# Kernel tuning notes

Hardware: AMD Instinct MI355X
Metric: run time of the kernel (lower is better)

## Reference

```python
import jax, jax.numpy as jnp
import numpy as np

N = 100000
E = 3200000
F_IN = 512
NUM_CLASSES = 8
H1, C1 = 4, 8   # conv1: 4 heads, 8 channels each (concat -> 32)
H2, C2 = 1, NUM_CLASSES  # conv2: 1 head, mean (concat=False)
NEG_SLOPE = 0.2


def gat_conv(x, W, att_src, att_dst, bias, src, dst, num_nodes, concat):
    """PyG-style GATConv (eval mode, self-loops already in src/dst)."""
    H, C = att_src.shape
    xp = (x @ W).reshape(-1, H, C)              # [N, H, C]
    a_s = (xp * att_src[None]).sum(-1)           # [N, H]
    a_d = (xp * att_dst[None]).sum(-1)           # [N, H]
    e = jax.nn.leaky_relu(a_s[src] + a_d[dst], NEG_SLOPE)  # [E, H]
    # segment softmax over destination nodes (stable)
    e_max = jax.ops.segment_max(e, dst, num_segments=num_nodes)
    e = jnp.exp(e - e_max[dst])
    denom = jax.ops.segment_sum(e, dst, num_segments=num_nodes)
    alpha = e / denom[dst]                        # [E, H]
    msg = xp[src] * alpha[..., None]              # [E, H, C]
    out = jax.ops.segment_sum(msg, dst, num_segments=num_nodes)  # [N, H, C]
    if concat:
        out = out.reshape(num_nodes, H * C)
    else:
        out = out.mean(axis=1)
    return out + bias


def setup_inputs() -> dict:
    key = jax.random.key(0)
    ks = jax.random.split(key, 9)
    s = 0.1
    return {
        "x": jax.random.normal(ks[0], (N, F_IN), dtype=jnp.float32),
        "edge_index": jax.random.randint(ks[1], (2, E), 0, N, dtype=jnp.int32),
        "W1": jax.random.normal(ks[2], (F_IN, H1 * C1), dtype=jnp.float32) * s,
        "att_src1": jax.random.normal(ks[3], (H1, C1), dtype=jnp.float32) * s,
        "att_dst1": jax.random.normal(ks[4], (H1, C1), dtype=jnp.float32) * s,
        "b1": jnp.zeros((H1 * C1,), dtype=jnp.float32),
        "W2": jax.random.normal(ks[5], (H1 * C1, H2 * C2), dtype=jnp.float32) * s,
        "att_src2": jax.random.normal(ks[6], (H2, C2), dtype=jnp.float32) * s,
        "att_dst2": jax.random.normal(ks[7], (H2, C2), dtype=jnp.float32) * s,
        "b2": jnp.zeros((C2,), dtype=jnp.float32),
    }


def reference(x, edge_index, W1, att_src1, att_dst1, b1, W2, att_src2, att_dst2, b2):
    # PyG GATConv default add_self_loops=True
    loop = jnp.arange(N, dtype=edge_index.dtype)
    src = jnp.concatenate([edge_index[0], loop])
    dst = jnp.concatenate([edge_index[1], loop])
    # dropout is identity in eval mode
    h = jax.nn.elu(gat_conv(x, W1, att_src1, att_dst1, b1, src, dst, N, True))
    out = gat_conv(h, W2, att_src2, att_dst2, b2, src, dst, N, False)
    return out
```

## Files before the change

kernel.cpp:

```cpp
#include <hip/hip_runtime.h>

typedef unsigned short u16;
typedef unsigned int   u32;

#define NN  100000
#define EE  3200000
#define ETOT 3300000
#define FIN 512
#define NBUK 512
#define NPB  196
#define TILE_A 8192
#define NBLK_A ((ETOT + TILE_A - 1) / TILE_A)

typedef __attribute__((ext_vector_type(8))) short bfx8;
typedef __attribute__((ext_vector_type(4))) float f32x4;

__device__ __forceinline__ float bf2f(u16 u){ return __uint_as_float(((u32)u) << 16); }
__device__ __forceinline__ float lo16f(u32 v){ return __uint_as_float(v << 16); }
__device__ __forceinline__ float hi16f(u32 v){ return __uint_as_float(v & 0xffff0000u); }
__device__ __forceinline__ u16 f2bf(float f){
  u32 u = __float_as_uint(f);
  u += 0x7fffu + ((u >> 16) & 1u);
  return (u16)(u >> 16);
}
__device__ __forceinline__ u32 pack2(float a, float b){
  return ((u32)f2bf(b) << 16) | (u32)f2bf(a);
}


__global__ void __launch_bounds__(256) k_bcnt(const int* __restrict__ ei,
                                              u32* __restrict__ bcnt){
  __shared__ u32 h[NBUK];
  int t = threadIdx.x;
  h[t] = 0; h[t + 256] = 0;
  __syncthreads();
  int stride = gridDim.x * 256;
  for (int e = blockIdx.x*256 + t; e < ETOT; e += stride){
    int d = (e < EE) ? ei[EE + e] : (e - EE);
    atomicAdd(&h[(u32)d / NPB], 1u);
  }
  __syncthreads();
  u32 v0 = h[t], v1 = h[t + 256];
  if (v0) atomicAdd(&bcnt[t], v0);
  if (v1) atomicAdd(&bcnt[t + 256], v1);
}

__global__ void __launch_bounds__(512) k_bscan(const u32* __restrict__ bcnt,
                                               u32* __restrict__ bbase,
                                               u32* __restrict__ gcur,
                                               int* __restrict__ indptr){
  __shared__ u32 sd[512];
  int t = threadIdx.x;
  u32 v = bcnt[t];
  sd[t] = v; __syncthreads();
  for (int o = 1; o < 512; o <<= 1){
    u32 x = (t >= o) ? sd[t - o] : 0;
    __syncthreads();
    sd[t] += x;
    __syncthreads();
  }
  u32 excl = sd[t] - v;
  bbase[t] = excl; gcur[t] = excl;
  if (t == 511) bbase[512] = sd[511];
  if (t == 0)   indptr[NN] = ETOT;
}

__global__ void __launch_bounds__(256) k_binA(const int* __restrict__ ei,
                                              u32* __restrict__ gcur,
                                              u32* __restrict__ buk){
  __shared__ u32 hcnt[NBUK];
  __shared__ u32 hbase[NBUK];
  int t = threadIdx.x;
  hcnt[t] = 0; hcnt[t + 256] = 0;
  __syncthreads();
  int e0 = blockIdx.x * TILE_A;
  u32 pk[32], meta[32];
  #pragma unroll
  for (int i = 0; i < 32; i++){
    int e = e0 + i*256 + t;
    if (e < ETOT){
      int s, d;
      if (e < EE){ s = ei[e]; d = ei[EE + e]; } else { s = e - EE; d = s; }
      u32 b = (u32)d / NPB;
      pk[i] = ((u32)(d - (int)b*NPB) << 17) | (u32)s;
      u32 r = atomicAdd(&hcnt[b], 1u);
      meta[i] = (b << 13) | r;
    } else meta[i] = 0xFFFFFFFFu;
  }
  __syncthreads();
  for (int q = t; q < NBUK; q += 256){
    u32 c = hcnt[q];
    if (c) hbase[q] = atomicAdd(&gcur[q], c);
  }
  __syncthreads();
  #pragma unroll
  for (int i = 0; i < 32; i++){
    if (meta[i] != 0xFFFFFFFFu){
      u32 b = meta[i] >> 13, r = meta[i] & 8191u;
      buk[hbase[b] + r] = pk[i];
    }
  }
}

__global__ void __launch_bounds__(256) k_scatterB(const u32* __restrict__ bbase,
                                                  const u32* __restrict__ buk,
                                                  int* __restrict__ indptr,
                                                  int* __restrict__ srcs){
  __shared__ u32 dcnt[NPB + 1];
  __shared__ u32 cur[NPB];
  int b = blockIdx.x, t = threadIdx.x;
  u32 lo = bbase[b], hi = bbase[b + 1];
  if (t < NPB + 1) dcnt[t] = 0;
  __syncthreads();
  for (u32 j = lo + t; j < hi; j += 256)
    atomicAdd(&dcnt[(buk[j] >> 17) + 1], 1u);
  __syncthreads();
  for (int o = 1; o < 256; o <<= 1){
    u32 x = 0;
    if (t < NPB + 1 && t >= o) x = dcnt[t - o];
    __syncthreads();
    if (t < NPB + 1 && t >= o) dcnt[t] += x;
    __syncthreads();
  }
  if (t < NPB){
    u32 off = lo + dcnt[t];
    cur[t] = off;
    int node = b * NPB + t;
    if (node < NN) indptr[node] = (int)off;
  }
  __syncthreads();
  for (u32 j = lo + t; j < hi; j += 256){
    u32 p = buk[j];
    u32 pos = atomicAdd(&cur[p >> 17], 1u);
    srcs[pos] = (int)(p & 0x1FFFFu);
  }
}


__global__ void k_prep_w(const float* __restrict__ W1, u16* __restrict__ WTb){
  int i = blockIdx.x*blockDim.x + threadIdx.x;
  if (i >= FIN*32) return;
  int k = i >> 5, c = i & 31;
  WTb[c*FIN + k] = f2bf(W1[i]);
}

__global__ void __launch_bounds__(256) k_gemm1(
    const float* __restrict__ x, const u16* __restrict__ WTb,
    const float* __restrict__ attS, const float* __restrict__ attD,
    u16* __restrict__ xp1, float* __restrict__ as1, float* __restrict__ ad1){
  __shared__ u16 xs[64 * 136];
  __shared__ u16 ws[32 * 520];
  int tid = threadIdx.x;
  int nb  = blockIdx.x * 64;

  {
    int r = tid >> 3, seg = tid & 7;
    const uint4* src = (const uint4*)(WTb + r*FIN + seg*64);
    uint4* dst = (uint4*)(ws + r*520 + seg*64);
    #pragma unroll
    for (int i = 0; i < 8; i++) dst[i] = src[i];
  }

  int sr = tid >> 2, sseg = tid & 3;
  int rowc = nb + sr; if (rowc >= NN) rowc = NN - 1;
  const float* xrow = x + (size_t)rowc * FIN;

  int lane = tid & 63, wid = tid >> 6;
  int m = lane & 15, quad = lane >> 4;
  int rowbase = wid * 16;
  const u16* a_base  = xs + (rowbase + m) * 136 + quad * 8;
  const u16* b0_base = ws + m * 520 + quad * 8;
  const u16* b1_base = b0_base + 16 * 520;

  f32x4 acc0 = {0.f, 0.f, 0.f, 0.f};
  f32x4 acc1 = {0.f, 0.f, 0.f, 0.f};

  for (int kc = 0; kc < 4; kc++){
    const float4* g = (const float4*)(xrow + kc*128 + sseg*32);
    #pragma unroll
    for (int i = 0; i < 4; i++){
      float4 f0 = g[2*i], f1 = g[2*i+1];
      uint4 wv;
      wv.x = pack2(f0.x, f0.y); wv.y = pack2(f0.z, f0.w);
      wv.z = pack2(f1.x, f1.y); wv.w = pack2(f1.z, f1.w);
      *(uint4*)(xs + sr*136 + sseg*32 + i*8) = wv;
    }
    __syncthreads();
    #pragma unroll
    for (int ks = 0; ks < 4; ks++){
      bfx8 a  = *(const bfx8*)(a_base + ks*32);
      bfx8 b0 = *(const bfx8*)(b0_base + kc*128 + ks*32);
      bfx8 b1 = *(const bfx8*)(b1_base + kc*128 + ks*32);
      acc0 = __builtin_amdgcn_mfma_f32_16x16x32_bf16(a, b0, acc0, 0, 0, 0);
      acc1 = __builtin_amdgcn_mfma_f32_16x16x32_bf16(a, b1, acc1, 0, 0, 0);
    }
    __syncthreads();
  }

  #pragma unroll
  for (int t = 0; t < 2; t++){
    f32x4 acc = t ? acc1 : acc0;
    int colg = t*16 + m;
    float aS = attS[colg], aD = attD[colg];
    #pragma unroll
    for (int r = 0; r < 4; r++){
      int node = nb + rowbase + quad*4 + r;
      float v = acc[r];
      if (node < NN) xp1[(size_t)node*32 + colg] = f2bf(v);
      float ps = v * aS, pd = v * aD;
      ps += __shfl_xor(ps, 1); ps += __shfl_xor(ps, 2); ps += __shfl_xor(ps, 4);
      pd += __shfl_xor(pd, 1); pd += __shfl_xor(pd, 2); pd += __shfl_xor(pd, 4);
      if ((m & 7) == 0 && node < NN){
        as1[node*4 + (colg >> 3)] = ps;
        ad1[node*4 + (colg >> 3)] = pd;
      }
    }
  }
}

__global__ void __launch_bounds__(256) k_agg1(
    const int* __restrict__ indptr, const int* __restrict__ srcs,
    const u32* __restrict__ xp1u, const float* __restrict__ as1,
    const float* __restrict__ ad1, const float* __restrict__ b1,
    u32* __restrict__ hfeatu){
  int wid = (blockIdx.x * 256 + threadIdx.x) >> 6;
  if (wid >= NN) return;
  int lane = threadIdx.x & 63;
  int e = lane >> 4;
  int l = lane & 15;
  int h = l >> 2;
  int beg = indptr[wid], end = indptr[wid + 1];
  float ad = ad1[wid*4 + h];
  float num0 = 0.f, num1 = 0.f, den = 0.f;
  int j = beg + e;
  for (; j + 4 < end; j += 8){
    int s0 = srcs[j], s1 = srcs[j + 4];
    u32 v0 = xp1u[(size_t)s0*16 + l];
    u32 v1 = xp1u[(size_t)s1*16 + l];
    float z0 = as1[s0*4 + h] + ad;
    float z1 = as1[s1*4 + h] + ad;
    z0 = (z0 >= 0.f) ? z0 : 0.2f * z0;
    z1 = (z1 >= 0.f) ? z1 : 0.2f * z1;
    float w0 = __expf(z0), w1 = __expf(z1);
    num0 = fmaf(w0, lo16f(v0), num0); num1 = fmaf(w0, hi16f(v0), num1); den += w0;
    num0 = fmaf(w1, lo16f(v1), num0); num1 = fmaf(w1, hi16f(v1), num1); den += w1;
  }
  for (; j < end; j += 4){
    int s0 = srcs[j];
    u32 v0 = xp1u[(size_t)s0*16 + l];
    float z0 = as1[s0*4 + h] + ad;
    z0 = (z0 >= 0.f) ? z0 : 0.2f * z0;
    float w0 = __expf(z0);
    num0 = fmaf(w0, lo16f(v0), num0); num1 = fmaf(w0, hi16f(v0), num1); den += w0;
  }
  num0 += __shfl_xor(num0, 16); num0 += __shfl_xor(num0, 32);
  num1 += __shfl_xor(num1, 16); num1 += __shfl_xor(num1, 32);
  den  += __shfl_xor(den, 16);  den  += __shfl_xor(den, 32);
  if (e == 0){
    float o0 = num0 / den + b1[2*l];
    float o1 = num1 / den + b1[2*l + 1];
    o0 = (o0 > 0.f) ? o0 : (__expf(o0) - 1.f);
    o1 = (o1 > 0.f) ? o1 : (__expf(o1) - 1.f);
    hfeatu[(size_t)wid*16 + l] = pack2(o0, o1);
  }
}

__global__ void k_feat2(const u16* __restrict__ hfeat, const float* __restrict__ W2,
                        const float* __restrict__ attS, const float* __restrict__ attD,
                        float* __restrict__ xp2, float* __restrict__ as2,
                        float* __restrict__ ad2){
  int n = blockIdx.x*blockDim.x + threadIdx.x;
  if (n >= NN) return;
  const u16* hr = hfeat + (size_t)n*32;
  float h[32];
  #pragma unroll
  for (int k = 0; k < 32; k++) h[k] = bf2f(hr[k]);
  float o[8];
  #pragma unroll
  for (int j = 0; j < 8; j++) o[j] = 0.f;
  #pragma unroll
  for (int k = 0; k < 32; k++){
    #pragma unroll
    for (int j = 0; j < 8; j++) o[j] = fmaf(h[k], W2[k*8 + j], o[j]);
  }
  float s = 0.f, d = 0.f;
  #pragma unroll
  for (int j = 0; j < 8; j++){
    xp2[(size_t)n*8 + j] = o[j];
    s = fmaf(o[j], attS[j], s);
    d = fmaf(o[j], attD[j], d);
  }
  as2[n] = s; ad2[n] = d;
}

__global__ void __launch_bounds__(256) k_agg2(
    const int* __restrict__ indptr, const int* __restrict__ srcs,
    const float* __restrict__ xp2, const float* __restrict__ as2,
    const float* __restrict__ ad2, const float* __restrict__ b2,
    float* __restrict__ out){
  int wid = (blockIdx.x * 256 + threadIdx.x) >> 6;
  if (wid >= NN) return;
  int lane = threadIdx.x & 63;
  int p = lane >> 3, c = lane & 7;
  int beg = indptr[wid], end = indptr[wid + 1];
  float ad = ad2[wid];
  float num = 0.f, den = 0.f;
  int j = beg + p;
  for (; j + 8 < end; j += 16){
    int s0 = srcs[j], s1 = srcs[j + 8];
    float v0 = xp2[(size_t)s0*8 + c];
    float v1 = xp2[(size_t)s1*8 + c];
    float z0 = as2[s0] + ad;
    float z1 = as2[s1] + ad;
    z0 = (z0 >= 0.f) ? z0 : 0.2f * z0;
    z1 = (z1 >= 0.f) ? z1 : 0.2f * z1;
    float w0 = __expf(z0), w1 = __expf(z1);
    num = fmaf(w0, v0, num); den += w0;
    num = fmaf(w1, v1, num); den += w1;
  }
  for (; j < end; j += 8){
    int s0 = srcs[j];
    float v0 = xp2[(size_t)s0*8 + c];
    float z0 = as2[s0] + ad;
    z0 = (z0 >= 0.f) ? z0 : 0.2f * z0;
    float w0 = __expf(z0);
    num = fmaf(w0, v0, num); den += w0;
  }
  num += __shfl_xor(num, 8);  den += __shfl_xor(den, 8);
  num += __shfl_xor(num, 16); den += __shfl_xor(den, 16);
  num += __shfl_xor(num, 32); den += __shfl_xor(den, 32);
  if (p == 0){
    out[(size_t)wid*8 + c] = num / den + b2[c];
  }
}

extern "C" void kernel_launch(void* const* d_in, const int* in_sizes, int n_in,
                              void* d_out, int out_size, void* d_ws, size_t ws_size,
                              hipStream_t stream){
  (void)in_sizes; (void)n_in; (void)out_size; (void)ws_size;
  const float* x   = (const float*)d_in[0];
  const int*   ei  = (const int*)d_in[1];
  const float* W1  = (const float*)d_in[2];
  const float* aS1 = (const float*)d_in[3];
  const float* aD1 = (const float*)d_in[4];
  const float* b1  = (const float*)d_in[5];
  const float* W2  = (const float*)d_in[6];
  const float* aS2 = (const float*)d_in[7];
  const float* aD2 = (const float*)d_in[8];
  const float* b2  = (const float*)d_in[9];
  float* out = (float*)d_out;

  char* w = (char*)d_ws;
  int*   indptr = (int*)w;   w += 400016;
  int*   srcs   = (int*)w;   w += (size_t)ETOT*4;
  u16*   xp1    = (u16*)w;   w += (size_t)NN*32*2;
  float* as1    = (float*)w; w += (size_t)NN*4*4;
  float* ad1    = (float*)w; w += (size_t)NN*4*4;
  u16*   hfeat  = (u16*)w;   w += (size_t)NN*32*2;
  float* xp2    = (float*)w; w += (size_t)NN*8*4;
  float* as2    = (float*)w; w += (size_t)NN*4;
  float* ad2    = (float*)w; w += (size_t)NN*4;
  u16*   WTb    = (u16*)w;   w += 32*512*2;
  u32*   bcnt   = (u32*)w;   w += NBUK*4;
  u32*   bbase  = (u32*)w;   w += (NBUK+1)*4 + 12;
  u32*   gcur   = (u32*)w;   w += NBUK*4;
  u32*   buk    = (u32*)xp1;

  hipMemsetAsync(bcnt, 0, NBUK*4, stream);
  k_bcnt    <<<256, 256, 0, stream>>>(ei, bcnt);
  k_bscan   <<<1, 512, 0, stream>>>(bcnt, bbase, gcur, indptr);
  k_binA    <<<NBLK_A, 256, 0, stream>>>(ei, gcur, buk);
  k_scatterB<<<NBUK, 256, 0, stream>>>(bbase, buk, indptr, srcs);
  k_prep_w  <<<64, 256, 0, stream>>>(W1, WTb);
  k_gemm1   <<<(NN+63)/64, 256, 0, stream>>>(x, WTb, aS1, aD1, xp1, as1, ad1);
  k_agg1    <<<NN/4, 256, 0, stream>>>(indptr, srcs, (const u32*)xp1, as1, ad1, b1, (u32*)hfeat);
  k_feat2   <<<(NN+255)/256, 256, 0, stream>>>(hfeat, W2, aS2, aD2, xp2, as2, ad2);
  k_agg2    <<<NN/4, 256, 0, stream>>>(indptr, srcs, xp2, as2, ad2, b2, out);
}
```

Before: 542.4 us.

## Fuse layer-2 projection into layer-1 aggregation and unroll gather loops

Folds the k_feat2 kernel into the epilogue of k_agg1, so each wave computes the ELU output, multiplies it by W2 with a shuffle reduction, and writes xp2 and the attention logits directly. The attention-weighted W2 vectors are precomputed in k_prep_w. This drops the hfeat round trip and one kernel launch. The gather loops in both aggregation kernels are also unrolled to four edges per iteration, with nontemporal loads on srcs, to raise memory-level parallelism. In exchange the layer-2 features now come from fp32 instead of bf16-rounded hidden values, and the agg1 epilogue gains extra shuffles.

```diff
diff --git a/kernel.cpp b/kernel.cpp
--- a/kernel.cpp
+++ b/kernel.cpp
@@ -137,8 +137,21 @@
 }
 
 
-__global__ void k_prep_w(const float* __restrict__ W1, u16* __restrict__ WTb){
+__global__ void k_prep_w(const float* __restrict__ W1, const float* __restrict__ W2,
+                         const float* __restrict__ aS2, const float* __restrict__ aD2,
+                         u16* __restrict__ WTb, float* __restrict__ wS2,
+                         float* __restrict__ wD2){
   int i = blockIdx.x*blockDim.x + threadIdx.x;
+  if (i < 32){
+    float s = 0.f, d = 0.f;
+    #pragma unroll
+    for (int j = 0; j < 8; j++){
+      float w = W2[i*8 + j];
+      s = fmaf(w, aS2[j], s);
+      d = fmaf(w, aD2[j], d);
+    }
+    wS2[i] = s; wD2[i] = d;
+  }
   if (i >= FIN*32) return;
   int k = i >> 5, c = i & 31;
   WTb[c*FIN + k] = f2bf(W1[i]);
@@ -222,7 +235,9 @@
     const int* __restrict__ indptr, const int* __restrict__ srcs,
     const u32* __restrict__ xp1u, const float* __restrict__ as1,
     const float* __restrict__ ad1, const float* __restrict__ b1,
-    u32* __restrict__ hfeatu){
+    const float* __restrict__ W2, const float* __restrict__ wS2,
+    const float* __restrict__ wD2,
+    float* __restrict__ xp2, float* __restrict__ as2, float* __restrict__ ad2){
   int wid = (blockIdx.x * 256 + threadIdx.x) >> 6;
   if (wid >= NN) return;
   int lane = threadIdx.x & 63;
@@ -233,8 +248,32 @@
   float ad = ad1[wid*4 + h];
   float num0 = 0.f, num1 = 0.f, den = 0.f;
   int j = beg + e;
-  for (; j + 4 < end; j += 8){
-    int s0 = srcs[j], s1 = srcs[j + 4];
+  for (; j + 12 < end; j += 16){
+    int s0 = __builtin_nontemporal_load(srcs + j);
+    int s1 = __builtin_nontemporal_load(srcs + j + 4);
+    int s2 = __builtin_nontemporal_load(srcs + j + 8);
+    int s3 = __builtin_nontemporal_load(srcs + j + 12);
+    u32 v0 = xp1u[(size_t)s0*16 + l];
+    u32 v1 = xp1u[(size_t)s1*16 + l];
+    u32 v2 = xp1u[(size_t)s2*16 + l];
+    u32 v3 = xp1u[(size_t)s3*16 + l];
+    float z0 = as1[s0*4 + h] + ad;
+    float z1 = as1[s1*4 + h] + ad;
+    float z2 = as1[s2*4 + h] + ad;
+    float z3 = as1[s3*4 + h] + ad;
+    z0 = (z0 >= 0.f) ? z0 : 0.2f * z0;
+    z1 = (z1 >= 0.f) ? z1 : 0.2f * z1;
+    z2 = (z2 >= 0.f) ? z2 : 0.2f * z2;
+    z3 = (z3 >= 0.f) ? z3 : 0.2f * z3;
+    float w0 = __expf(z0), w1 = __expf(z1), w2 = __expf(z2), w3 = __expf(z3);
+    num0 = fmaf(w0, lo16f(v0), num0); num1 = fmaf(w0, hi16f(v0), num1); den += w0;
+    num0 = fmaf(w1, lo16f(v1), num0); num1 = fmaf(w1, hi16f(v1), num1); den += w1;
+    num0 = fmaf(w2, lo16f(v2), num0); num1 = fmaf(w2, hi16f(v2), num1); den += w2;
+    num0 = fmaf(w3, lo16f(v3), num0); num1 = fmaf(w3, hi16f(v3), num1); den += w3;
+  }
+  if (j + 4 < end){
+    int s0 = __builtin_nontemporal_load(srcs + j);
+    int s1 = __builtin_nontemporal_load(srcs + j + 4);
     u32 v0 = xp1u[(size_t)s0*16 + l];
     u32 v1 = xp1u[(size_t)s1*16 + l];
     float z0 = as1[s0*4 + h] + ad;
@@ -244,9 +283,10 @@
     float w0 = __expf(z0), w1 = __expf(z1);
     num0 = fmaf(w0, lo16f(v0), num0); num1 = fmaf(w0, hi16f(v0), num1); den += w0;
     num0 = fmaf(w1, lo16f(v1), num0); num1 = fmaf(w1, hi16f(v1), num1); den += w1;
+    j += 8;
   }
   for (; j < end; j += 4){
-    int s0 = srcs[j];
+    int s0 = __builtin_nontemporal_load(srcs + j);
     u32 v0 = xp1u[(size_t)s0*16 + l];
     float z0 = as1[s0*4 + h] + ad;
     z0 = (z0 >= 0.f) ? z0 : 0.2f * z0;
@@ -257,40 +297,41 @@
   num1 += __shfl_xor(num1, 16); num1 += __shfl_xor(num1, 32);
   den  += __shfl_xor(den, 16);  den  += __shfl_xor(den, 32);
   if (e == 0){
-    float o0 = num0 / den + b1[2*l];
-    float o1 = num1 / den + b1[2*l + 1];
-    o0 = (o0 > 0.f) ? o0 : (__expf(o0) - 1.f);
-    o1 = (o1 > 0.f) ? o1 : (__expf(o1) - 1.f);
-    hfeatu[(size_t)wid*16 + l] = pack2(o0, o1);
-  }
-}
-
-__global__ void k_feat2(const u16* __restrict__ hfeat, const float* __restrict__ W2,
-                        const float* __restrict__ attS, const float* __restrict__ attD,
-                        float* __restrict__ xp2, float* __restrict__ as2,
-                        float* __restrict__ ad2){
-  int n = blockIdx.x*blockDim.x + threadIdx.x;
-  if (n >= NN) return;
-  const u16* hr = hfeat + (size_t)n*32;
-  float h[32];
-  #pragma unroll
-  for (int k = 0; k < 32; k++) h[k] = bf2f(hr[k]);
-  float o[8];
-  #pragma unroll
-  for (int j = 0; j < 8; j++) o[j] = 0.f;
-  #pragma unroll
-  for (int k = 0; k < 32; k++){
-    #pragma unroll
-    for (int j = 0; j < 8; j++) o[j] = fmaf(h[k], W2[k*8 + j], o[j]);
-  }
-  float s = 0.f, d = 0.f;
-  #pragma unroll
-  for (int j = 0; j < 8; j++){
-    xp2[(size_t)n*8 + j] = o[j];
-    s = fmaf(o[j], attS[j], s);
-    d = fmaf(o[j], attD[j], d);
-  }
-  as2[n] = s; ad2[n] = d;
+    float h0 = num0 / den + b1[2*l];
+    float h1 = num1 / den + b1[2*l + 1];
+    h0 = (h0 > 0.f) ? h0 : (__expf(h0) - 1.f);
+    h1 = (h1 > 0.f) ? h1 : (__expf(h1) - 1.f);
+    float p0 = 0.f, p1 = 0.f, p2 = 0.f, p3 = 0.f;
+    float p4 = 0.f, p5 = 0.f, p6 = 0.f, p7 = 0.f;
+    const float* wr0 = W2 + (2*l)*8;
+    const float* wr1 = W2 + (2*l+1)*8;
+    p0 = fmaf(h0, wr0[0], h1*wr1[0]);
+    p1 = fmaf(h0, wr0[1], h1*wr1[1]);
+    p2 = fmaf(h0, wr0[2], h1*wr1[2]);
+    p3 = fmaf(h0, wr0[3], h1*wr1[3]);
+    p4 = fmaf(h0, wr0[4], h1*wr1[4]);
+    p5 = fmaf(h0, wr0[5], h1*wr1[5]);
+    p6 = fmaf(h0, wr0[6], h1*wr1[6]);
+    p7 = fmaf(h0, wr0[7], h1*wr1[7]);
+    float ps = fmaf(h0, wS2[2*l], h1*wS2[2*l+1]);
+    float pd = fmaf(h0, wD2[2*l], h1*wD2[2*l+1]);
+    #pragma unroll
+    for (int mm = 1; mm <= 8; mm <<= 1){
+      p0 += __shfl_xor(p0, mm); p1 += __shfl_xor(p1, mm);
+      p2 += __shfl_xor(p2, mm); p3 += __shfl_xor(p3, mm);
+      p4 += __shfl_xor(p4, mm); p5 += __shfl_xor(p5, mm);
+      p6 += __shfl_xor(p6, mm); p7 += __shfl_xor(p7, mm);
+      ps += __shfl_xor(ps, mm); pd += __shfl_xor(pd, mm);
+    }
+    if (l < 8){
+      float o = p0;
+      o = (l == 1) ? p1 : o; o = (l == 2) ? p2 : o; o = (l == 3) ? p3 : o;
+      o = (l == 4) ? p4 : o; o = (l == 5) ? p5 : o; o = (l == 6) ? p6 : o;
+      o = (l == 7) ? p7 : o;
+      xp2[(size_t)wid*8 + l] = o;
+    }
+    if (l == 0){ as2[wid] = ps; ad2[wid] = pd; }
+  }
 }
 
 __global__ void __launch_bounds__(256) k_agg2(
@@ -306,8 +347,32 @@
   float ad = ad2[wid];
   float num = 0.f, den = 0.f;
   int j = beg + p;
-  for (; j + 8 < end; j += 16){
-    int s0 = srcs[j], s1 = srcs[j + 8];
+  for (; j + 24 < end; j += 32){
+    int s0 = __builtin_nontemporal_load(srcs + j);
+    int s1 = __builtin_nontemporal_load(srcs + j + 8);
+    int s2 = __builtin_nontemporal_load(srcs + j + 16);
+    int s3 = __builtin_nontemporal_load(srcs + j + 24);
+    float v0 = xp2[(size_t)s0*8 + c];
+    float v1 = xp2[(size_t)s1*8 + c];
+    float v2 = xp2[(size_t)s2*8 + c];
+    float v3 = xp2[(size_t)s3*8 + c];
+    float z0 = as2[s0] + ad;
+    float z1 = as2[s1] + ad;
+    float z2 = as2[s2] + ad;
+    float z3 = as2[s3] + ad;
+    z0 = (z0 >= 0.f) ? z0 : 0.2f * z0;
+    z1 = (z1 >= 0.f) ? z1 : 0.2f * z1;
+    z2 = (z2 >= 0.f) ? z2 : 0.2f * z2;
+    z3 = (z3 >= 0.f) ? z3 : 0.2f * z3;
+    float w0 = __expf(z0), w1 = __expf(z1), w2 = __expf(z2), w3 = __expf(z3);
+    num = fmaf(w0, v0, num); den += w0;
+    num = fmaf(w1, v1, num); den += w1;
+    num = fmaf(w2, v2, num); den += w2;
+    num = fmaf(w3, v3, num); den += w3;
+  }
+  if (j + 8 < end){
+    int s0 = __builtin_nontemporal_load(srcs + j);
+    int s1 = __builtin_nontemporal_load(srcs + j + 8);
     float v0 = xp2[(size_t)s0*8 + c];
     float v1 = xp2[(size_t)s1*8 + c];
     float z0 = as2[s0] + ad;
@@ -317,9 +382,10 @@
     float w0 = __expf(z0), w1 = __expf(z1);
     num = fmaf(w0, v0, num); den += w0;
     num = fmaf(w1, v1, num); den += w1;
+    j += 16;
   }
   for (; j < end; j += 8){
-    int s0 = srcs[j];
+    int s0 = __builtin_nontemporal_load(srcs + j);
     float v0 = xp2[(size_t)s0*8 + c];
     float z0 = as2[s0] + ad;
     z0 = (z0 >= 0.f) ? z0 : 0.2f * z0;
@@ -356,11 +422,13 @@
   u16*   xp1    = (u16*)w;   w += (size_t)NN*32*2;
   float* as1    = (float*)w; w += (size_t)NN*4*4;
   float* ad1    = (float*)w; w += (size_t)NN*4*4;
-  u16*   hfeat  = (u16*)w;   w += (size_t)NN*32*2;
+  w += (size_t)NN*32*2;
   float* xp2    = (float*)w; w += (size_t)NN*8*4;
   float* as2    = (float*)w; w += (size_t)NN*4;
   float* ad2    = (float*)w; w += (size_t)NN*4;
   u16*   WTb    = (u16*)w;   w += 32*512*2;
+  float* wS2    = (float*)w; w += 32*4;
+  float* wD2    = (float*)w; w += 32*4;
   u32*   bcnt   = (u32*)w;   w += NBUK*4;
   u32*   bbase  = (u32*)w;   w += (NBUK+1)*4 + 12;
   u32*   gcur   = (u32*)w;   w += NBUK*4;
@@ -371,9 +439,9 @@
   k_bscan   <<<1, 512, 0, stream>>>(bcnt, bbase, gcur, indptr);
   k_binA    <<<NBLK_A, 256, 0, stream>>>(ei, gcur, buk);
   k_scatterB<<<NBUK, 256, 0, stream>>>(bbase, buk, indptr, srcs);
-  k_prep_w  <<<64, 256, 0, stream>>>(W1, WTb);
+  k_prep_w  <<<64, 256, 0, stream>>>(W1, W2, aS2, aD2, WTb, wS2, wD2);
   k_gemm1   <<<(NN+63)/64, 256, 0, stream>>>(x, WTb, aS1, aD1, xp1, as1, ad1);
-  k_agg1    <<<NN/4, 256, 0, stream>>>(indptr, srcs, (const u32*)xp1, as1, ad1, b1, (u32*)hfeat);
-  k_feat2   <<<(NN+255)/256, 256, 0, stream>>>(hfeat, W2, aS2, aD2, xp2, as2, ad2);
+  k_agg1    <<<NN/4, 256, 0, stream>>>(indptr, srcs, (const u32*)xp1, as1, ad1, b1,
+                                       W2, wS2, wD2, xp2, as2, ad2);
   k_agg2    <<<NN/4, 256, 0, stream>>>(indptr, srcs, xp2, as2, ad2, b2, out);
 }
```

After: 559.6 us. +3.2%, slower.

## Drop edge counting pass with fixed-capacity buckets and load GEMM A directly

Applied to the files above, without the earlier changes.

The separate destination-histogram kernel is removed. Edges are now binned into fixed-capacity (8192-slot) buckets, counted atomically during binning, and prefix-summed afterwards. The compact indptr array is replaced by per-node (begin,end) int2 ranges written by the scatter kernel. Separately, the first GEMM no longer stages x through LDS; each lane loads its fp32 A fragment straight from global memory and converts it to bf16 in registers, which removes the per-chunk barriers. The costs are a larger scratch footprint, silent corruption if any bucket exceeds its capacity, and less coalesced global loads in the GEMM.

```diff
diff --git a/kernel.cpp b/kernel.cpp
--- a/kernel.cpp
+++ b/kernel.cpp
@@ -9,6 +9,7 @@
 #define FIN 512
 #define NBUK 512
 #define NPB  196
+#define CAP  8192
 #define TILE_A 8192
 #define NBLK_A ((ETOT + TILE_A - 1) / TILE_A)
 
@@ -28,45 +29,8 @@
 }
 
 
-__global__ void __launch_bounds__(256) k_bcnt(const int* __restrict__ ei,
-                                              u32* __restrict__ bcnt){
-  __shared__ u32 h[NBUK];
-  int t = threadIdx.x;
-  h[t] = 0; h[t + 256] = 0;
-  __syncthreads();
-  int stride = gridDim.x * 256;
-  for (int e = blockIdx.x*256 + t; e < ETOT; e += stride){
-    int d = (e < EE) ? ei[EE + e] : (e - EE);
-    atomicAdd(&h[(u32)d / NPB], 1u);
-  }
-  __syncthreads();
-  u32 v0 = h[t], v1 = h[t + 256];
-  if (v0) atomicAdd(&bcnt[t], v0);
-  if (v1) atomicAdd(&bcnt[t + 256], v1);
-}
-
-__global__ void __launch_bounds__(512) k_bscan(const u32* __restrict__ bcnt,
-                                               u32* __restrict__ bbase,
-                                               u32* __restrict__ gcur,
-                                               int* __restrict__ indptr){
-  __shared__ u32 sd[512];
-  int t = threadIdx.x;
-  u32 v = bcnt[t];
-  sd[t] = v; __syncthreads();
-  for (int o = 1; o < 512; o <<= 1){
-    u32 x = (t >= o) ? sd[t - o] : 0;
-    __syncthreads();
-    sd[t] += x;
-    __syncthreads();
-  }
-  u32 excl = sd[t] - v;
-  bbase[t] = excl; gcur[t] = excl;
-  if (t == 511) bbase[512] = sd[511];
-  if (t == 0)   indptr[NN] = ETOT;
-}
-
 __global__ void __launch_bounds__(256) k_binA(const int* __restrict__ ei,
-                                              u32* __restrict__ gcur,
+                                              u32* __restrict__ gcnt,
                                               u32* __restrict__ buk){
   __shared__ u32 hcnt[NBUK];
   __shared__ u32 hbase[NBUK];
@@ -90,26 +54,44 @@
   __syncthreads();
   for (int q = t; q < NBUK; q += 256){
     u32 c = hcnt[q];
-    if (c) hbase[q] = atomicAdd(&gcur[q], c);
+    if (c) hbase[q] = atomicAdd(&gcnt[q], c);
   }
   __syncthreads();
   #pragma unroll
   for (int i = 0; i < 32; i++){
     if (meta[i] != 0xFFFFFFFFu){
       u32 b = meta[i] >> 13, r = meta[i] & 8191u;
-      buk[hbase[b] + r] = pk[i];
+      buk[((u32)b << 13) + hbase[b] + r] = pk[i];
     }
   }
 }
 
-__global__ void __launch_bounds__(256) k_scatterB(const u32* __restrict__ bbase,
+__global__ void __launch_bounds__(512) k_bscan(const u32* __restrict__ gcnt,
+                                               u32* __restrict__ sbase){
+  __shared__ u32 sd[512];
+  int t = threadIdx.x;
+  u32 v = gcnt[t];
+  sd[t] = v; __syncthreads();
+  for (int o = 1; o < 512; o <<= 1){
+    u32 x = (t >= o) ? sd[t - o] : 0;
+    __syncthreads();
+    sd[t] += x;
+    __syncthreads();
+  }
+  sbase[t] = sd[t] - v;
+}
+
+__global__ void __launch_bounds__(256) k_scatterB(const u32* __restrict__ gcnt,
+                                                  const u32* __restrict__ sbase,
                                                   const u32* __restrict__ buk,
-                                                  int* __restrict__ indptr,
+                                                  int2* __restrict__ range,
                                                   int* __restrict__ srcs){
   __shared__ u32 dcnt[NPB + 1];
   __shared__ u32 cur[NPB];
   int b = blockIdx.x, t = threadIdx.x;
-  u32 lo = bbase[b], hi = bbase[b + 1];
+  u32 lo = (u32)b << 13;
+  u32 hi = lo + gcnt[b];
+  u32 gb = sbase[b];
   if (t < NPB + 1) dcnt[t] = 0;
   __syncthreads();
   for (u32 j = lo + t; j < hi; j += 256)
@@ -123,10 +105,13 @@
     __syncthreads();
   }
   if (t < NPB){
-    u32 off = lo + dcnt[t];
-    cur[t] = off;
+    u32 beg = gb + dcnt[t];
+    cur[t] = beg;
     int node = b * NPB + t;
-    if (node < NN) indptr[node] = (int)off;
+    if (node < NN){
+      u32 end = gb + dcnt[t + 1];
+      range[node] = make_int2((int)beg, (int)end);
+    }
   }
   __syncthreads();
   for (u32 j = lo + t; j < hi; j += 256){
@@ -148,7 +133,6 @@
     const float* __restrict__ x, const u16* __restrict__ WTb,
     const float* __restrict__ attS, const float* __restrict__ attD,
     u16* __restrict__ xp1, float* __restrict__ as1, float* __restrict__ ad1){
-  __shared__ u16 xs[64 * 136];
   __shared__ u16 ws[32 * 520];
   int tid = threadIdx.x;
   int nb  = blockIdx.x * 64;
@@ -160,41 +144,35 @@
     #pragma unroll
     for (int i = 0; i < 8; i++) dst[i] = src[i];
   }
-
-  int sr = tid >> 2, sseg = tid & 3;
-  int rowc = nb + sr; if (rowc >= NN) rowc = NN - 1;
-  const float* xrow = x + (size_t)rowc * FIN;
+  __syncthreads();
 
   int lane = tid & 63, wid = tid >> 6;
   int m = lane & 15, quad = lane >> 4;
   int rowbase = wid * 16;
-  const u16* a_base  = xs + (rowbase + m) * 136 + quad * 8;
+  int row = nb + rowbase + m; if (row >= NN) row = NN - 1;
+  const float* xrow = x + (size_t)row * FIN + quad * 8;
   const u16* b0_base = ws + m * 520 + quad * 8;
   const u16* b1_base = b0_base + 16 * 520;
 
   f32x4 acc0 = {0.f, 0.f, 0.f, 0.f};
   f32x4 acc1 = {0.f, 0.f, 0.f, 0.f};
 
+  union Ubf { bfx8 v; u32 u[4]; };
+
+  #pragma unroll
   for (int kc = 0; kc < 4; kc++){
-    const float4* g = (const float4*)(xrow + kc*128 + sseg*32);
-    #pragma unroll
-    for (int i = 0; i < 4; i++){
-      float4 f0 = g[2*i], f1 = g[2*i+1];
-      uint4 wv;
-      wv.x = pack2(f0.x, f0.y); wv.y = pack2(f0.z, f0.w);
-      wv.z = pack2(f1.x, f1.y); wv.w = pack2(f1.z, f1.w);
-      *(uint4*)(xs + sr*136 + sseg*32 + i*8) = wv;
-    }
-    __syncthreads();
     #pragma unroll
     for (int ks = 0; ks < 4; ks++){
-      bfx8 a  = *(const bfx8*)(a_base + ks*32);
+      const float4* g = (const float4*)(xrow + kc*128 + ks*32);
+      float4 f0 = g[0], f1 = g[1];
+      Ubf ua;
+      ua.u[0] = pack2(f0.x, f0.y); ua.u[1] = pack2(f0.z, f0.w);
+      ua.u[2] = pack2(f1.x, f1.y); ua.u[3] = pack2(f1.z, f1.w);
       bfx8 b0 = *(const bfx8*)(b0_base + kc*128 + ks*32);
       bfx8 b1 = *(const bfx8*)(b1_base + kc*128 + ks*32);
-      acc0 = __builtin_amdgcn_mfma_f32_16x16x32_bf16(a, b0, acc0, 0, 0, 0);
-      acc1 = __builtin_amdgcn_mfma_f32_16x16x32_bf16(a, b1, acc1, 0, 0, 0);
+      acc0 = __builtin_amdgcn_mfma_f32_16x16x32_bf16(ua.v, b0, acc0, 0, 0, 0);
+      acc1 = __builtin_amdgcn_mfma_f32_16x16x32_bf16(ua.v, b1, acc1, 0, 0, 0);
     }
-    __syncthreads();
   }
 
   #pragma unroll
@@ -219,7 +197,7 @@
 }
 
 __global__ void __launch_bounds__(256) k_agg1(
-    const int* __restrict__ indptr, const int* __restrict__ srcs,
+    const int2* __restrict__ range, const int* __restrict__ srcs,
     const u32* __restrict__ xp1u, const float* __restrict__ as1,
     const float* __restrict__ ad1, const float* __restrict__ b1,
     u32* __restrict__ hfeatu){
@@ -229,7 +207,8 @@
   int e = lane >> 4;
   int l = lane & 15;
   int h = l >> 2;
-  int beg = indptr[wid], end = indptr[wid + 1];
+  int2 rr = range[wid];
+  int beg = rr.x, end = rr.y;
   float ad = ad1[wid*4 + h];
   float num0 = 0.f, num1 = 0.f, den = 0.f;
   int j = beg + e;
@@ -294,7 +273,7 @@
 }
 
 __global__ void __launch_bounds__(256) k_agg2(
-    const int* __restrict__ indptr, const int* __restrict__ srcs,
+    const int2* __restrict__ range, const int* __restrict__ srcs,
     const float* __restrict__ xp2, const float* __restrict__ as2,
     const float* __restrict__ ad2, const float* __restrict__ b2,
     float* __restrict__ out){
@@ -302,7 +281,8 @@
   if (wid >= NN) return;
   int lane = threadIdx.x & 63;
   int p = lane >> 3, c = lane & 7;
-  int beg = indptr[wid], end = indptr[wid + 1];
+  int2 rr = range[wid];
+  int beg = rr.x, end = rr.y;
   float ad = ad2[wid];
   float num = 0.f, den = 0.f;
   int j = beg + p;
@@ -351,7 +331,7 @@
   float* out = (float*)d_out;
 
   char* w = (char*)d_ws;
-  int*   indptr = (int*)w;   w += 400016;
+  int2*  range  = (int2*)w;  w += (size_t)NN*8;
   int*   srcs   = (int*)w;   w += (size_t)ETOT*4;
   u16*   xp1    = (u16*)w;   w += (size_t)NN*32*2;
   float* as1    = (float*)w; w += (size_t)NN*4*4;
@@ -361,19 +341,17 @@
   float* as2    = (float*)w; w += (size_t)NN*4;
   float* ad2    = (float*)w; w += (size_t)NN*4;
   u16*   WTb    = (u16*)w;   w += 32*512*2;
-  u32*   bcnt   = (u32*)w;   w += NBUK*4;
-  u32*   bbase  = (u32*)w;   w += (NBUK+1)*4 + 12;
-  u32*   gcur   = (u32*)w;   w += NBUK*4;
+  u32*   gcnt   = (u32*)w;   w += NBUK*4;
+  u32*   sbase  = (u32*)w;   w += NBUK*4;
   u32*   buk    = (u32*)xp1;
 
-  hipMemsetAsync(bcnt, 0, NBUK*4, stream);
-  k_bcnt    <<<256, 256, 0, stream>>>(ei, bcnt);
-  k_bscan   <<<1, 512, 0, stream>>>(bcnt, bbase, gcur, indptr);
-  k_binA    <<<NBLK_A, 256, 0, stream>>>(ei, gcur, buk);
-  k_scatterB<<<NBUK, 256, 0, stream>>>(bbase, buk, indptr, srcs);
+  hipMemsetAsync(gcnt, 0, NBUK*4, stream);
+  k_binA    <<<NBLK_A, 256, 0, stream>>>(ei, gcnt, buk);
+  k_bscan   <<<1, 512, 0, stream>>>(gcnt, sbase);
+  k_scatterB<<<NBUK, 256, 0, stream>>>(gcnt, sbase, buk, range, srcs);
   k_prep_w  <<<64, 256, 0, stream>>>(W1, WTb);
   k_gemm1   <<<(NN+63)/64, 256, 0, stream>>>(x, WTb, aS1, aD1, xp1, as1, ad1);
-  k_agg1    <<<NN/4, 256, 0, stream>>>(indptr, srcs, (const u32*)xp1, as1, ad1, b1, (u32*)hfeat);
+  k_agg1    <<<NN/4, 256, 0, stream>>>(range, srcs, (const u32*)xp1, as1, ad1, b1, (u32*)hfeat);
   k_feat2   <<<(NN+255)/256, 256, 0, stream>>>(hfeat, W2, aS2, aD2, xp2, as2, ad2);
-  k_agg2    <<<NN/4, 256, 0, stream>>>(indptr, srcs, xp2, as2, ad2, b2, out);
-}
+  k_agg2    <<<NN/4, 256, 0, stream>>>(range, srcs, xp2, as2, ad2, b2, out);
+}
```

Result: faster. 506.1 us (-6.7%).
